# Kernel tuning notes

Hardware: AMD Instinct MI355X
Metric: run time of the kernel (lower is better)

The kernel has to match this reference:

```python
import jax, jax.numpy as jnp
import numpy as np

N_NODES = 20000
N_REL = 200
DIM = 128
N_EDGES = 200000
N_TIMES = 8


def setup_inputs() -> dict:
    key = jax.random.key(0)
    ks = jax.random.split(key, 12)
    s = 1.0 / np.sqrt(DIM)
    return {
        "edge_index": jax.random.randint(ks[0], (2, N_EDGES), 0, N_NODES),
        "edge_type": jax.random.randint(ks[1], (N_EDGES,), 0, N_REL),
        "edge_time": jax.random.randint(ks[2], (N_EDGES,), 0, N_TIMES),
        "edge_weight": jax.random.uniform(ks[3], (N_EDGES,), dtype=jnp.float32),
        "node_emb": jax.random.normal(ks[4], (N_NODES, DIM), dtype=jnp.float32),
        "rel_emb": jax.random.normal(ks[5], (N_REL, DIM), dtype=jnp.float32),
        "W_enc": jax.random.normal(ks[6], (DIM, DIM), dtype=jnp.float32) * s,
        "Wz": jax.random.normal(ks[7], (DIM, DIM), dtype=jnp.float32) * s,
        "Uz": jax.random.normal(ks[8], (DIM, DIM), dtype=jnp.float32) * s,
        "Wh": jax.random.normal(ks[9], (DIM, DIM), dtype=jnp.float32) * s,
        "Uh": jax.random.normal(ks[10], (DIM, DIM), dtype=jnp.float32) * s,
        "bz": jnp.zeros((DIM,), dtype=jnp.float32),
        "bh": jnp.zeros((DIM,), dtype=jnp.float32),
        "num_times": N_TIMES,
    }


def reference(edge_index, edge_type, edge_time, edge_weight,
              node_emb, rel_emb, W_enc, Wz, Uz, Wh, Uh, bz, bh, num_times):
    # TemporalEncoder.forward: loop over sorted unique timestamps; per-step
    # masked-edge GNN encode (R-GCN lite) then gated SSM cell; state detached.
    src, dst = edge_index[0], edge_index[1]
    rel_e = rel_emb[edge_type]          # [E, D] gather (constant across steps)
    src_e = node_emb[src]               # [E, D]
    n_nodes = node_emb.shape[0]

    def step(state, t):
        m = (edge_time == t).astype(edge_weight.dtype)       # [E]
        msg = src_e * rel_e * (edge_weight * m)[:, None]     # [E, D]
        agg = jax.ops.segment_sum(msg, dst, num_segments=n_nodes)  # [N, D]
        h = jnp.tanh(agg @ W_enc)                            # base_encoder output
        z = jax.nn.sigmoid(h @ Wz + state @ Uz + bz)
        cand = jnp.tanh(h @ Wh + state @ Uh + bh)
        new_state = (1.0 - z) * state + z * cand             # ssm.cell
        return jax.lax.stop_gradient(new_state), new_state   # state.detach()

    state0 = jnp.zeros_like(node_emb)
    _, outs = jax.lax.scan(step, state0, jnp.arange(num_times))
    return outs[-1]  # last_out, shape [N, D]
```

## Files before the change

kernel.cpp:

```cpp
#include <hip/hip_runtime.h>

#define N_NODES 20000
#define N_REL 200
#define N_EDGES 200000
#define DIM 128
#define T_STEPS 8
#define N_TILES (N_NODES / 16)
#define KEYS (N_NODES * T_STEPS)
#define SCAN_N (KEYS + 1)
#define SCAN_BLKS ((SCAN_N + 1023) / 1024)

typedef short short8 __attribute__((ext_vector_type(8)));
typedef float f32x4 __attribute__((ext_vector_type(4)));

static __device__ __forceinline__ unsigned short f2bf(float f) {
  union { float f; unsigned u; } v; v.f = f;
  unsigned r = v.u + 0x7fffu + ((v.u >> 16) & 1u);
  return (unsigned short)(r >> 16);
}
static __device__ __forceinline__ unsigned cvt_pk_bf16(float lo, float hi) {
  unsigned r;
  asm("v_cvt_pk_bf16_f32 %0, %1, %2" : "=v"(r) : "v"(lo), "v"(hi));
  return r;
}
static __device__ __forceinline__ float fast_tanh(float x) {
  float e = __expf(2.f * x);
  return 1.f - 2.f / (e + 1.f);
}
static __device__ __forceinline__ float fast_sig(float x) {
  return 1.f / (1.f + __expf(-x));
}

__global__ void repack5(const float* __restrict__ w0,
                        const float* __restrict__ w1,
                        const float* __restrict__ w2,
                        const float* __restrict__ w3,
                        const float* __restrict__ w4,
                        unsigned short* __restrict__ pack) {
  int i = blockIdx.x * blockDim.x + threadIdx.x;
  if (i >= 5 * 16384) return;
  int m = i >> 14, r = i & 16383;
  int j = r & 7, lane = (r >> 3) & 63, ks = (r >> 9) & 3, nt = (r >> 11) & 7;
  int n = nt * 16 + (lane & 15);
  int k = ks * 32 + (lane >> 4) * 8 + j;
  const float* w = (m == 0) ? w0 : (m == 1) ? w1 : (m == 2) ? w2
                 : (m == 3) ? w3 : w4;
  pack[i] = f2bf(w[k * DIM + n]);
}

__global__ void hist_k(const int* __restrict__ dst, const int* __restrict__ etime,
                       int* __restrict__ counts) {
  int i = blockIdx.x * blockDim.x + threadIdx.x;
  if (i >= N_EDGES) return;
  atomicAdd(&counts[dst[i] * T_STEPS + etime[i]], 1);
}

__global__ void scan1_k(const int* __restrict__ counts,
                        int* __restrict__ base, int* __restrict__ bsum) {
  __shared__ int ls[256];
  int tid = threadIdx.x;
  int i0 = blockIdx.x * 1024 + tid * 4;
  int v[4], ts = 0;
#pragma unroll
  for (int r = 0; r < 4; r++) {
    v[r] = (i0 + r < SCAN_N) ? counts[i0 + r] : 0;
    ts += v[r];
  }
  ls[tid] = ts; __syncthreads();
#pragma unroll
  for (int off = 1; off < 256; off <<= 1) {
    int x = (tid >= off) ? ls[tid - off] : 0;
    __syncthreads(); ls[tid] += x; __syncthreads();
  }
  int run = ls[tid] - ts;
  if (tid == 255) bsum[blockIdx.x] = ls[255];
#pragma unroll
  for (int r = 0; r < 4; r++) {
    if (i0 + r < SCAN_N) base[i0 + r] = run;
    run += v[r];
  }
}

__global__ void scan2_k(int* __restrict__ bsum) {
  __shared__ int ls[256];
  int tid = threadIdx.x;
  int v = (tid < SCAN_BLKS) ? bsum[tid] : 0;
  ls[tid] = v; __syncthreads();
#pragma unroll
  for (int off = 1; off < 256; off <<= 1) {
    int x = (tid >= off) ? ls[tid - off] : 0;
    __syncthreads(); ls[tid] += x; __syncthreads();
  }
  if (tid < SCAN_BLKS) bsum[tid] = ls[tid] - v;
}

__global__ void fill_k(const int* __restrict__ src, const int* __restrict__ dst,
                       const int* __restrict__ etype, const int* __restrict__ etime,
                       const float* __restrict__ ew,
                       const int* __restrict__ base, const int* __restrict__ bsum,
                       int* __restrict__ cursor, uint2* __restrict__ ep2) {
  int i = blockIdx.x * blockDim.x + threadIdx.x;
  if (i >= N_EDGES) return;
  int key = dst[i] * T_STEPS + etime[i];
  int pos = base[key] + bsum[key >> 10] + atomicAdd(&cursor[key], 1);
  uint2 e;
  e.x = (unsigned)src[i] | ((unsigned)etype[i] << 15);
  e.y = __float_as_uint(ew[i]);
  ep2[pos] = e;
}

__launch_bounds__(512, 4)
__global__ void fused_recur(const int* __restrict__ base,
                            const int* __restrict__ bsum,
                            const uint2* __restrict__ ep2,
                            const float* __restrict__ nemb,
                            const float* __restrict__ remb,
                            const unsigned short* __restrict__ pack,
                            const float* __restrict__ bz,
                            const float* __restrict__ bh,
                            float* __restrict__ out) {
  __shared__ unsigned short aggL[T_STEPS * 16 * 136];
  __shared__ unsigned short Hb[2][16 * 136];
  __shared__ unsigned short Sb[2][16 * 136];
  int lane = threadIdx.x & 63;
  int nt = threadIdx.x >> 6;
  int q = lane >> 4, l15 = lane & 15;
  int row0 = blockIdx.x * 16;
  int c = nt * 16 + l15;

#pragma unroll
  for (int ln = 0; ln < 2; ln++) {
    int nl = nt * 2 + ln;
    int kb = (row0 + nl) * T_STEPS;
    int prev = base[kb] + bsum[kb >> 10];
#pragma unroll
    for (int tt = 0; tt < T_STEPS; tt++) {
      int kn = kb + tt + 1;
      int e1 = base[kn] + bsum[kn >> 10];
      float ax = 0.f, ay = 0.f;
      for (int i = prev; i < e1; i++) {
        uint2 e = ep2[i];
        float w = __uint_as_float(e.y);
        int s = e.x & 0x7fff, rt = e.x >> 15;
        float2 sv = ((const float2*)(nemb + (size_t)s * DIM))[lane];
        float2 rv = ((const float2*)(remb + (size_t)rt * DIM))[lane];
        ax += sv.x * rv.x * w;
        ay += sv.y * rv.y * w;
      }
      prev = e1;
      ((unsigned*)&aggL[(tt * 16 + nl) * 136])[lane] = cvt_pk_bf16(ax, ay);
    }
  }
  __syncthreads();

  unsigned hpk[T_STEPS][2];
  {
    short8 wenc[4];
#pragma unroll
    for (int ks = 0; ks < 4; ks++)
      wenc[ks] = *(const short8*)(pack + ((nt * 4 + ks) * 64 + lane) * 8);
#pragma unroll
    for (int t = 0; t < T_STEPS; t++) {
      f32x4 acch = (f32x4){0.f, 0.f, 0.f, 0.f};
#pragma unroll
      for (int ks = 0; ks < 4; ks++) {
        short8 aA = *(const short8*)&aggL[(t * 16 + l15) * 136 + ks * 32 + q * 8];
        acch = __builtin_amdgcn_mfma_f32_16x16x32_bf16(aA, wenc[ks], acch, 0, 0, 0);
      }
      hpk[t][0] = cvt_pk_bf16(fast_tanh(acch[0]), fast_tanh(acch[1]));
      hpk[t][1] = cvt_pk_bf16(fast_tanh(acch[2]), fast_tanh(acch[3]));
    }
  }

  short8 wz[4], uz[4], wh[4], uh[4];
#pragma unroll
  for (int ks = 0; ks < 4; ks++) {
    int fo = ((nt * 4 + ks) * 64 + lane) * 8;
    wz[ks] = *(const short8*)(pack + 16384 * 1 + fo);
    uz[ks] = *(const short8*)(pack + 16384 * 2 + fo);
    wh[ks] = *(const short8*)(pack + 16384 * 3 + fo);
    uh[ks] = *(const short8*)(pack + 16384 * 4 + fo);
  }
  float bzv = bz[c];
  float bhv = bh[c];

  f32x4 stC = (f32x4){0.f, 0.f, 0.f, 0.f};

#pragma unroll
  for (int t = 0; t < T_STEPS; t++) {
    unsigned short* hB = Hb[t & 1];
    unsigned short* sB = Sb[t & 1];
    unsigned s01 = cvt_pk_bf16(stC[0], stC[1]);
    unsigned s23 = cvt_pk_bf16(stC[2], stC[3]);
    hB[(q * 4 + 0) * 136 + c] = (unsigned short)hpk[t][0];
    hB[(q * 4 + 1) * 136 + c] = (unsigned short)(hpk[t][0] >> 16);
    hB[(q * 4 + 2) * 136 + c] = (unsigned short)hpk[t][1];
    hB[(q * 4 + 3) * 136 + c] = (unsigned short)(hpk[t][1] >> 16);
    sB[(q * 4 + 0) * 136 + c] = (unsigned short)s01;
    sB[(q * 4 + 1) * 136 + c] = (unsigned short)(s01 >> 16);
    sB[(q * 4 + 2) * 136 + c] = (unsigned short)s23;
    sB[(q * 4 + 3) * 136 + c] = (unsigned short)(s23 >> 16);
    __syncthreads();

    f32x4 accz = (f32x4){bzv, bzv, bzv, bzv};
    f32x4 accc = (f32x4){bhv, bhv, bhv, bhv};
#pragma unroll
    for (int ks = 0; ks < 4; ks++) {
      short8 hA = *(const short8*)&hB[l15 * 136 + ks * 32 + q * 8];
      short8 sA = *(const short8*)&sB[l15 * 136 + ks * 32 + q * 8];
      accz = __builtin_amdgcn_mfma_f32_16x16x32_bf16(hA, wz[ks], accz, 0, 0, 0);
      accz = __builtin_amdgcn_mfma_f32_16x16x32_bf16(sA, uz[ks], accz, 0, 0, 0);
      accc = __builtin_amdgcn_mfma_f32_16x16x32_bf16(hA, wh[ks], accc, 0, 0, 0);
      accc = __builtin_amdgcn_mfma_f32_16x16x32_bf16(sA, uh[ks], accc, 0, 0, 0);
    }
#pragma unroll
    for (int r = 0; r < 4; r++) {
      float z = fast_sig(accz[r]);
      float cc = fast_tanh(accc[r]);
      stC[r] = (1.f - z) * stC[r] + z * cc;
    }
  }

#pragma unroll
  for (int r = 0; r < 4; r++)
    out[(size_t)(row0 + q * 4 + r) * DIM + c] = stC[r];
}

extern "C" void kernel_launch(void* const* d_in, const int* in_sizes, int n_in,
                              void* d_out, int out_size, void* d_ws, size_t ws_size,
                              hipStream_t stream) {
  const int* eidx  = (const int*)d_in[0];
  const int* src   = eidx;
  const int* dst   = eidx + N_EDGES;
  const int* etype = (const int*)d_in[1];
  const int* etime = (const int*)d_in[2];
  const float* ew   = (const float*)d_in[3];
  const float* nemb = (const float*)d_in[4];
  const float* remb = (const float*)d_in[5];
  const float* Wenc = (const float*)d_in[6];
  const float* Wz   = (const float*)d_in[7];
  const float* Uz   = (const float*)d_in[8];
  const float* Wh   = (const float*)d_in[9];
  const float* Uh   = (const float*)d_in[10];
  const float* bz   = (const float*)d_in[11];
  const float* bh   = (const float*)d_in[12];

  int* counts = (int*)d_ws;
  int* cursor = counts + SCAN_N;
  int* bsum   = cursor + KEYS;
  int* base   = bsum + 256;
  uint2* ep2  = (uint2*)(base + ((SCAN_N + 1) & ~1));
  unsigned short* pack = (unsigned short*)(ep2 + N_EDGES);
  float* outp = (float*)d_out;

  hipMemsetAsync(counts, 0, (size_t)(SCAN_N + KEYS) * sizeof(int), stream);
  repack5<<<(5 * 16384 + 255) / 256, 256, 0, stream>>>(Wenc, Wz, Uz, Wh, Uh, pack);
  hist_k<<<(N_EDGES + 255) / 256, 256, 0, stream>>>(dst, etime, counts);
  scan1_k<<<SCAN_BLKS, 256, 0, stream>>>(counts, base, bsum);
  scan2_k<<<1, 256, 0, stream>>>(bsum);
  fill_k<<<(N_EDGES + 255) / 256, 256, 0, stream>>>(src, dst, etype, etime, ew,
                                                    base, bsum, cursor, ep2);
  fused_recur<<<N_TILES, 512, 0, stream>>>(base, bsum, ep2, nemb, remb,
                                           pack, bz, bh, outp);
}
```

Baseline: 213.1 us.

## Replace CSR sort with fixed-capacity per-tile edge buckets

Drops the histogram, two-level scan and sorted fill, replacing them with one atomic append of each edge into a fixed 512-slot bucket per 16-node tile, with time and local row packed into the edge word. The recurrence kernel now scans the whole tile bucket in every wave, skips edges that belong to other waves, and accumulates into per-timestep register arrays through predicated adds. This removes the memset and several launch and scan passes. In exchange every wave reads all edges of its tile and keeps more registers live, and edges beyond the capacity are silently dropped, which only works if no tile exceeds 512 edges (the mean here is about 160).

```diff
diff --git a/kernel.cpp b/kernel.cpp
--- a/kernel.cpp
+++ b/kernel.cpp
@@ -6,9 +6,7 @@
 #define DIM 128
 #define T_STEPS 8
 #define N_TILES (N_NODES / 16)
-#define KEYS (N_NODES * T_STEPS)
-#define SCAN_N (KEYS + 1)
-#define SCAN_BLKS ((SCAN_N + 1023) / 1024)
+#define CAP 512
 
 typedef short short8 __attribute__((ext_vector_type(8)));
 typedef float f32x4 __attribute__((ext_vector_type(4)));
@@ -36,8 +34,10 @@
                         const float* __restrict__ w2,
                         const float* __restrict__ w3,
                         const float* __restrict__ w4,
-                        unsigned short* __restrict__ pack) {
+                        unsigned short* __restrict__ pack,
+                        int* __restrict__ cursor) {
   int i = blockIdx.x * blockDim.x + threadIdx.x;
+  if (i < N_TILES) cursor[i] = 0;
   if (i >= 5 * 16384) return;
   int m = i >> 14, r = i & 16383;
   int j = r & 7, lane = (r >> 3) & 63, ks = (r >> 9) & 3, nt = (r >> 11) & 7;
@@ -48,71 +48,27 @@
   pack[i] = f2bf(w[k * DIM + n]);
 }
 
-__global__ void hist_k(const int* __restrict__ dst, const int* __restrict__ etime,
-                       int* __restrict__ counts) {
+__global__ void binfill_k(const int* __restrict__ src, const int* __restrict__ dst,
+                          const int* __restrict__ etype, const int* __restrict__ etime,
+                          const float* __restrict__ ew,
+                          int* __restrict__ cursor, uint2* __restrict__ bkt) {
   int i = blockIdx.x * blockDim.x + threadIdx.x;
   if (i >= N_EDGES) return;
-  atomicAdd(&counts[dst[i] * T_STEPS + etime[i]], 1);
-}
-
-__global__ void scan1_k(const int* __restrict__ counts,
-                        int* __restrict__ base, int* __restrict__ bsum) {
-  __shared__ int ls[256];
-  int tid = threadIdx.x;
-  int i0 = blockIdx.x * 1024 + tid * 4;
-  int v[4], ts = 0;
-#pragma unroll
-  for (int r = 0; r < 4; r++) {
-    v[r] = (i0 + r < SCAN_N) ? counts[i0 + r] : 0;
-    ts += v[r];
-  }
-  ls[tid] = ts; __syncthreads();
-#pragma unroll
-  for (int off = 1; off < 256; off <<= 1) {
-    int x = (tid >= off) ? ls[tid - off] : 0;
-    __syncthreads(); ls[tid] += x; __syncthreads();
-  }
-  int run = ls[tid] - ts;
-  if (tid == 255) bsum[blockIdx.x] = ls[255];
-#pragma unroll
-  for (int r = 0; r < 4; r++) {
-    if (i0 + r < SCAN_N) base[i0 + r] = run;
-    run += v[r];
-  }
-}
-
-__global__ void scan2_k(int* __restrict__ bsum) {
-  __shared__ int ls[256];
-  int tid = threadIdx.x;
-  int v = (tid < SCAN_BLKS) ? bsum[tid] : 0;
-  ls[tid] = v; __syncthreads();
-#pragma unroll
-  for (int off = 1; off < 256; off <<= 1) {
-    int x = (tid >= off) ? ls[tid - off] : 0;
-    __syncthreads(); ls[tid] += x; __syncthreads();
-  }
-  if (tid < SCAN_BLKS) bsum[tid] = ls[tid] - v;
-}
-
-__global__ void fill_k(const int* __restrict__ src, const int* __restrict__ dst,
-                       const int* __restrict__ etype, const int* __restrict__ etime,
-                       const float* __restrict__ ew,
-                       const int* __restrict__ base, const int* __restrict__ bsum,
-                       int* __restrict__ cursor, uint2* __restrict__ ep2) {
-  int i = blockIdx.x * blockDim.x + threadIdx.x;
-  if (i >= N_EDGES) return;
-  int key = dst[i] * T_STEPS + etime[i];
-  int pos = base[key] + bsum[key >> 10] + atomicAdd(&cursor[key], 1);
-  uint2 e;
-  e.x = (unsigned)src[i] | ((unsigned)etype[i] << 15);
-  e.y = __float_as_uint(ew[i]);
-  ep2[pos] = e;
+  int d = dst[i];
+  int tile = d >> 4;
+  int pos = atomicAdd(&cursor[tile], 1);
+  if (pos < CAP) {
+    uint2 e;
+    e.x = (unsigned)src[i] | ((unsigned)etype[i] << 15)
+        | ((unsigned)etime[i] << 23) | ((unsigned)(d & 15) << 26);
+    e.y = __float_as_uint(ew[i]);
+    bkt[(size_t)tile * CAP + pos] = e;
+  }
 }
 
 __launch_bounds__(512, 4)
-__global__ void fused_recur(const int* __restrict__ base,
-                            const int* __restrict__ bsum,
-                            const uint2* __restrict__ ep2,
+__global__ void fused_recur(const int* __restrict__ cursor,
+                            const uint2* __restrict__ bkt,
                             const float* __restrict__ nemb,
                             const float* __restrict__ remb,
                             const unsigned short* __restrict__ pack,
@@ -125,30 +81,46 @@
   int lane = threadIdx.x & 63;
   int nt = threadIdx.x >> 6;
   int q = lane >> 4, l15 = lane & 15;
-  int row0 = blockIdx.x * 16;
+  int tile = blockIdx.x;
+  int row0 = tile * 16;
   int c = nt * 16 + l15;
 
-#pragma unroll
-  for (int ln = 0; ln < 2; ln++) {
-    int nl = nt * 2 + ln;
-    int kb = (row0 + nl) * T_STEPS;
-    int prev = base[kb] + bsum[kb >> 10];
+  {
+    int cnt = cursor[tile];
+    if (cnt > CAP) cnt = CAP;
+    const uint2* bp = bkt + (size_t)tile * CAP;
+    float ax0[T_STEPS], ay0[T_STEPS], ax1[T_STEPS], ay1[T_STEPS];
 #pragma unroll
     for (int tt = 0; tt < T_STEPS; tt++) {
-      int kn = kb + tt + 1;
-      int e1 = base[kn] + bsum[kn >> 10];
-      float ax = 0.f, ay = 0.f;
-      for (int i = prev; i < e1; i++) {
-        uint2 e = ep2[i];
+      ax0[tt] = 0.f; ay0[tt] = 0.f; ax1[tt] = 0.f; ay1[tt] = 0.f;
+    }
+    for (int i = 0; i < cnt; i++) {
+      uint2 e = bp[i];
+      int nl = (int)(e.x >> 26);
+      if ((nl >> 1) == nt) {
+        int s = e.x & 0x7fff, rt = (e.x >> 15) & 0xff, t = (e.x >> 23) & 7;
         float w = __uint_as_float(e.y);
-        int s = e.x & 0x7fff, rt = e.x >> 15;
         float2 sv = ((const float2*)(nemb + (size_t)s * DIM))[lane];
         float2 rv = ((const float2*)(remb + (size_t)rt * DIM))[lane];
-        ax += sv.x * rv.x * w;
-        ay += sv.y * rv.y * w;
+        float m0 = sv.x * rv.x * w;
+        float m1 = sv.y * rv.y * w;
+        bool odd = nl & 1;
+        float e00 = odd ? 0.f : m0, e01 = odd ? 0.f : m1;
+        float e10 = odd ? m0 : 0.f, e11 = odd ? m1 : 0.f;
+#pragma unroll
+        for (int tt = 0; tt < T_STEPS; tt++) {
+          bool h = (t == tt);
+          ax0[tt] += h ? e00 : 0.f;
+          ay0[tt] += h ? e01 : 0.f;
+          ax1[tt] += h ? e10 : 0.f;
+          ay1[tt] += h ? e11 : 0.f;
+        }
       }
-      prev = e1;
-      ((unsigned*)&aggL[(tt * 16 + nl) * 136])[lane] = cvt_pk_bf16(ax, ay);
+    }
+#pragma unroll
+    for (int tt = 0; tt < T_STEPS; tt++) {
+      ((unsigned*)&aggL[(tt * 16 + nt * 2 + 0) * 136])[lane] = cvt_pk_bf16(ax0[tt], ay0[tt]);
+      ((unsigned*)&aggL[(tt * 16 + nt * 2 + 1) * 136])[lane] = cvt_pk_bf16(ax1[tt], ay1[tt]);
     }
   }
   __syncthreads();
@@ -245,21 +217,15 @@
   const float* bz   = (const float*)d_in[11];
   const float* bh   = (const float*)d_in[12];
 
-  int* counts = (int*)d_ws;
-  int* cursor = counts + SCAN_N;
-  int* bsum   = cursor + KEYS;
-  int* base   = bsum + 256;
-  uint2* ep2  = (uint2*)(base + ((SCAN_N + 1) & ~1));
-  unsigned short* pack = (unsigned short*)(ep2 + N_EDGES);
+  int* cursor = (int*)d_ws;
+  uint2* bkt  = (uint2*)(cursor + ((N_TILES + 1) & ~1));
+  unsigned short* pack = (unsigned short*)(bkt + (size_t)N_TILES * CAP);
   float* outp = (float*)d_out;
 
-  hipMemsetAsync(counts, 0, (size_t)(SCAN_N + KEYS) * sizeof(int), stream);
-  repack5<<<(5 * 16384 + 255) / 256, 256, 0, stream>>>(Wenc, Wz, Uz, Wh, Uh, pack);
-  hist_k<<<(N_EDGES + 255) / 256, 256, 0, stream>>>(dst, etime, counts);
-  scan1_k<<<SCAN_BLKS, 256, 0, stream>>>(counts, base, bsum);
-  scan2_k<<<1, 256, 0, stream>>>(bsum);
-  fill_k<<<(N_EDGES + 255) / 256, 256, 0, stream>>>(src, dst, etype, etime, ew,
-                                                    base, bsum, cursor, ep2);
-  fused_recur<<<N_TILES, 512, 0, stream>>>(base, bsum, ep2, nemb, remb,
+  repack5<<<(5 * 16384 + 255) / 256, 256, 0, stream>>>(Wenc, Wz, Uz, Wh, Uh,
+                                                       pack, cursor);
+  binfill_k<<<(N_EDGES + 255) / 256, 256, 0, stream>>>(src, dst, etype, etime,
+                                                       ew, cursor, bkt);
+  fused_recur<<<N_TILES, 512, 0, stream>>>(cursor, bkt, nemb, remb,
                                            pack, bz, bh, outp);
 }
```

New measurement: 239.0 us. +12.2%, slower.

## Interleave two node gathers per wavefront and split recurrent MFMA chains

Applied to the files above, without the earlier changes.

The edge-gather phase now preloads all CSR bounds for the wavefront's two nodes and walks both nodes' edge lists in one interleaved loop, so their independent global loads can be in flight together instead of running as two serial chains. The recurrent GRU step splits each gate accumulation into separate h-path and state-path accumulators, which shortens dependent MFMA chains. It also skips the state MFMAs, the state LDS stores and the state LDS reads at t=0, where the state is zero. The interleaved loop adds branch divergence when the two lists differ in length, and the extra accumulators raise register pressure.

```diff
diff --git a/kernel.cpp b/kernel.cpp
--- a/kernel.cpp
+++ b/kernel.cpp
@@ -125,30 +125,46 @@
   int lane = threadIdx.x & 63;
   int nt = threadIdx.x >> 6;
   int q = lane >> 4, l15 = lane & 15;
-  int row0 = blockIdx.x * 16;
+  int tile = blockIdx.x;
+  int row0 = tile * 16;
   int c = nt * 16 + l15;
 
-#pragma unroll
-  for (int ln = 0; ln < 2; ln++) {
-    int nl = nt * 2 + ln;
-    int kb = (row0 + nl) * T_STEPS;
-    int prev = base[kb] + bsum[kb >> 10];
+  {
+    int kb = (row0 + nt * 2) * T_STEPS;
+    int b0[9], b1[9];
+#pragma unroll
+    for (int k = 0; k < 9; k++) {
+      int k0 = kb + k, k1 = kb + T_STEPS + k;
+      b0[k] = base[k0] + bsum[k0 >> 10];
+      b1[k] = base[k1] + bsum[k1 >> 10];
+    }
+    int i0 = b0[0], i1 = b1[0];
 #pragma unroll
     for (int tt = 0; tt < T_STEPS; tt++) {
-      int kn = kb + tt + 1;
-      int e1 = base[kn] + bsum[kn >> 10];
-      float ax = 0.f, ay = 0.f;
-      for (int i = prev; i < e1; i++) {
-        uint2 e = ep2[i];
-        float w = __uint_as_float(e.y);
-        int s = e.x & 0x7fff, rt = e.x >> 15;
-        float2 sv = ((const float2*)(nemb + (size_t)s * DIM))[lane];
-        float2 rv = ((const float2*)(remb + (size_t)rt * DIM))[lane];
-        ax += sv.x * rv.x * w;
-        ay += sv.y * rv.y * w;
+      int e0 = b0[tt + 1], e1 = b1[tt + 1];
+      float ax0 = 0.f, ay0 = 0.f, ax1 = 0.f, ay1 = 0.f;
+      while (i0 < e0 || i1 < e1) {
+        if (i0 < e0) {
+          uint2 e = ep2[i0++];
+          float w = __uint_as_float(e.y);
+          int s = e.x & 0x7fff, rt = e.x >> 15;
+          float2 sv = ((const float2*)(nemb + (size_t)s * DIM))[lane];
+          float2 rv = ((const float2*)(remb + (size_t)rt * DIM))[lane];
+          ax0 += sv.x * rv.x * w;
+          ay0 += sv.y * rv.y * w;
+        }
+        if (i1 < e1) {
+          uint2 e = ep2[i1++];
+          float w = __uint_as_float(e.y);
+          int s = e.x & 0x7fff, rt = e.x >> 15;
+          float2 sv = ((const float2*)(nemb + (size_t)s * DIM))[lane];
+          float2 rv = ((const float2*)(remb + (size_t)rt * DIM))[lane];
+          ax1 += sv.x * rv.x * w;
+          ay1 += sv.y * rv.y * w;
+        }
       }
-      prev = e1;
-      ((unsigned*)&aggL[(tt * 16 + nl) * 136])[lane] = cvt_pk_bf16(ax, ay);
+      ((unsigned*)&aggL[(tt * 16 + nt * 2 + 0) * 136])[lane] = cvt_pk_bf16(ax0, ay0);
+      ((unsigned*)&aggL[(tt * 16 + nt * 2 + 1) * 136])[lane] = cvt_pk_bf16(ax1, ay1);
     }
   }
   __syncthreads();
@@ -190,33 +206,50 @@
   for (int t = 0; t < T_STEPS; t++) {
     unsigned short* hB = Hb[t & 1];
     unsigned short* sB = Sb[t & 1];
-    unsigned s01 = cvt_pk_bf16(stC[0], stC[1]);
-    unsigned s23 = cvt_pk_bf16(stC[2], stC[3]);
     hB[(q * 4 + 0) * 136 + c] = (unsigned short)hpk[t][0];
     hB[(q * 4 + 1) * 136 + c] = (unsigned short)(hpk[t][0] >> 16);
     hB[(q * 4 + 2) * 136 + c] = (unsigned short)hpk[t][1];
     hB[(q * 4 + 3) * 136 + c] = (unsigned short)(hpk[t][1] >> 16);
-    sB[(q * 4 + 0) * 136 + c] = (unsigned short)s01;
-    sB[(q * 4 + 1) * 136 + c] = (unsigned short)(s01 >> 16);
-    sB[(q * 4 + 2) * 136 + c] = (unsigned short)s23;
-    sB[(q * 4 + 3) * 136 + c] = (unsigned short)(s23 >> 16);
+    if (t > 0) {
+      unsigned s01 = cvt_pk_bf16(stC[0], stC[1]);
+      unsigned s23 = cvt_pk_bf16(stC[2], stC[3]);
+      sB[(q * 4 + 0) * 136 + c] = (unsigned short)s01;
+      sB[(q * 4 + 1) * 136 + c] = (unsigned short)(s01 >> 16);
+      sB[(q * 4 + 2) * 136 + c] = (unsigned short)s23;
+      sB[(q * 4 + 3) * 136 + c] = (unsigned short)(s23 >> 16);
+    }
     __syncthreads();
 
-    f32x4 accz = (f32x4){bzv, bzv, bzv, bzv};
-    f32x4 accc = (f32x4){bhv, bhv, bhv, bhv};
+    short8 hA[4], sA[4];
+#pragma unroll
+    for (int ks = 0; ks < 4; ks++)
+      hA[ks] = *(const short8*)&hB[l15 * 136 + ks * 32 + q * 8];
+    if (t > 0) {
+#pragma unroll
+      for (int ks = 0; ks < 4; ks++)
+        sA[ks] = *(const short8*)&sB[l15 * 136 + ks * 32 + q * 8];
+    }
+
+    f32x4 zh = (f32x4){bzv, bzv, bzv, bzv};
+    f32x4 ch = (f32x4){bhv, bhv, bhv, bhv};
+    f32x4 zs = (f32x4){0.f, 0.f, 0.f, 0.f};
+    f32x4 cs = (f32x4){0.f, 0.f, 0.f, 0.f};
 #pragma unroll
     for (int ks = 0; ks < 4; ks++) {
-      short8 hA = *(const short8*)&hB[l15 * 136 + ks * 32 + q * 8];
-      short8 sA = *(const short8*)&sB[l15 * 136 + ks * 32 + q * 8];
-      accz = __builtin_amdgcn_mfma_f32_16x16x32_bf16(hA, wz[ks], accz, 0, 0, 0);
-      accz = __builtin_amdgcn_mfma_f32_16x16x32_bf16(sA, uz[ks], accz, 0, 0, 0);
-      accc = __builtin_amdgcn_mfma_f32_16x16x32_bf16(hA, wh[ks], accc, 0, 0, 0);
-      accc = __builtin_amdgcn_mfma_f32_16x16x32_bf16(sA, uh[ks], accc, 0, 0, 0);
+      zh = __builtin_amdgcn_mfma_f32_16x16x32_bf16(hA[ks], wz[ks], zh, 0, 0, 0);
+      ch = __builtin_amdgcn_mfma_f32_16x16x32_bf16(hA[ks], wh[ks], ch, 0, 0, 0);
+    }
+    if (t > 0) {
+#pragma unroll
+      for (int ks = 0; ks < 4; ks++) {
+        zs = __builtin_amdgcn_mfma_f32_16x16x32_bf16(sA[ks], uz[ks], zs, 0, 0, 0);
+        cs = __builtin_amdgcn_mfma_f32_16x16x32_bf16(sA[ks], uh[ks], cs, 0, 0, 0);
+      }
     }
 #pragma unroll
     for (int r = 0; r < 4; r++) {
-      float z = fast_sig(accz[r]);
-      float cc = fast_tanh(accc[r]);
+      float z = fast_sig(zh[r] + zs[r]);
+      float cc = fast_tanh(ch[r] + cs[r]);
       stC[r] = (1.f - z) * stC[r] + z * cc;
     }
   }
```

Result: no change. 214.2 us (+0.5%).

## Precompute input-side gate projections for all steps outside the serial recurrence

Applied to the files above, without the earlier changes.

The h@Wz and h@Wh products for all timesteps are now computed in a batched pre-pass, with h stored back into the agg shared buffer, before the sequential state loop. The recurrent loop then only runs the state@Uz and state@Uh MFMAs. Step 0 is peeled because the state starts at zero, which removes its barrier and state MFMAs, and the separate H shared buffer is dropped. Keeping the precomputed accumulators in registers raises register pressure, so the occupancy hint falls from 4 to 3 blocks per CU.

```diff
diff --git a/kernel.cpp b/kernel.cpp
--- a/kernel.cpp
+++ b/kernel.cpp
@@ -109,7 +109,7 @@
   ep2[pos] = e;
 }
 
-__launch_bounds__(512, 4)
+__launch_bounds__(512, 3)
 __global__ void fused_recur(const int* __restrict__ base,
                             const int* __restrict__ bsum,
                             const uint2* __restrict__ ep2,
@@ -120,12 +120,12 @@
                             const float* __restrict__ bh,
                             float* __restrict__ out) {
   __shared__ unsigned short aggL[T_STEPS * 16 * 136];
-  __shared__ unsigned short Hb[2][16 * 136];
   __shared__ unsigned short Sb[2][16 * 136];
   int lane = threadIdx.x & 63;
   int nt = threadIdx.x >> 6;
   int q = lane >> 4, l15 = lane & 15;
-  int row0 = blockIdx.x * 16;
+  int tile = blockIdx.x;
+  int row0 = tile * 16;
   int c = nt * 16 + l15;
 
 #pragma unroll
@@ -171,52 +171,91 @@
       hpk[t][1] = cvt_pk_bf16(fast_tanh(acch[2]), fast_tanh(acch[3]));
     }
   }
-
-  short8 wz[4], uz[4], wh[4], uh[4];
+  __syncthreads();
+
+#pragma unroll
+  for (int t = 0; t < T_STEPS; t++) {
+    int rbase = (t * 16 + q * 4) * 136 + c;
+    aggL[rbase + 0 * 136] = (unsigned short)hpk[t][0];
+    aggL[rbase + 1 * 136] = (unsigned short)(hpk[t][0] >> 16);
+    aggL[rbase + 2 * 136] = (unsigned short)hpk[t][1];
+    aggL[rbase + 3 * 136] = (unsigned short)(hpk[t][1] >> 16);
+  }
+  __syncthreads();
+
+  f32x4 zh[T_STEPS], ch[T_STEPS];
+  {
+    short8 wzf[4], whf[4];
+#pragma unroll
+    for (int ks = 0; ks < 4; ks++) {
+      int fo = ((nt * 4 + ks) * 64 + lane) * 8;
+      wzf[ks] = *(const short8*)(pack + 16384 * 1 + fo);
+      whf[ks] = *(const short8*)(pack + 16384 * 3 + fo);
+    }
+    float bzv = bz[c];
+    float bhv = bh[c];
+#pragma unroll
+    for (int t = 0; t < T_STEPS; t++) {
+      short8 hA[4];
+#pragma unroll
+      for (int ks = 0; ks < 4; ks++)
+        hA[ks] = *(const short8*)&aggL[(t * 16 + l15) * 136 + ks * 32 + q * 8];
+      f32x4 az = (f32x4){bzv, bzv, bzv, bzv};
+      f32x4 ac = (f32x4){bhv, bhv, bhv, bhv};
+#pragma unroll
+      for (int ks = 0; ks < 4; ks++) {
+        az = __builtin_amdgcn_mfma_f32_16x16x32_bf16(hA[ks], wzf[ks], az, 0, 0, 0);
+        ac = __builtin_amdgcn_mfma_f32_16x16x32_bf16(hA[ks], whf[ks], ac, 0, 0, 0);
+      }
+      zh[t] = az;
+      ch[t] = ac;
+    }
+  }
+
+  short8 uz[4], uh[4];
 #pragma unroll
   for (int ks = 0; ks < 4; ks++) {
     int fo = ((nt * 4 + ks) * 64 + lane) * 8;
-    wz[ks] = *(const short8*)(pack + 16384 * 1 + fo);
     uz[ks] = *(const short8*)(pack + 16384 * 2 + fo);
-    wh[ks] = *(const short8*)(pack + 16384 * 3 + fo);
     uh[ks] = *(const short8*)(pack + 16384 * 4 + fo);
   }
-  float bzv = bz[c];
-  float bhv = bh[c];
-
-  f32x4 stC = (f32x4){0.f, 0.f, 0.f, 0.f};
-
-#pragma unroll
-  for (int t = 0; t < T_STEPS; t++) {
-    unsigned short* hB = Hb[t & 1];
+
+  f32x4 stC;
+#pragma unroll
+  for (int r = 0; r < 4; r++) {
+    float z = fast_sig(zh[0][r]);
+    float cc = fast_tanh(ch[0][r]);
+    stC[r] = z * cc;
+  }
+
+#pragma unroll
+  for (int t = 1; t < T_STEPS; t++) {
     unsigned short* sB = Sb[t & 1];
     unsigned s01 = cvt_pk_bf16(stC[0], stC[1]);
     unsigned s23 = cvt_pk_bf16(stC[2], stC[3]);
-    hB[(q * 4 + 0) * 136 + c] = (unsigned short)hpk[t][0];
-    hB[(q * 4 + 1) * 136 + c] = (unsigned short)(hpk[t][0] >> 16);
-    hB[(q * 4 + 2) * 136 + c] = (unsigned short)hpk[t][1];
-    hB[(q * 4 + 3) * 136 + c] = (unsigned short)(hpk[t][1] >> 16);
-    sB[(q * 4 + 0) * 136 + c] = (unsigned short)s01;
-    sB[(q * 4 + 1) * 136 + c] = (unsigned short)(s01 >> 16);
-    sB[(q * 4 + 2) * 136 + c] = (unsigned short)s23;
-    sB[(q * 4 + 3) * 136 + c] = (unsigned short)(s23 >> 16);
+    int rbase = (q * 4) * 136 + c;
+    sB[rbase + 0 * 136] = (unsigned short)s01;
+    sB[rbase + 1 * 136] = (unsigned short)(s01 >> 16);
+    sB[rbase + 2 * 136] = (unsigned short)s23;
+    sB[rbase + 3 * 136] = (unsigned short)(s23 >> 16);
     __syncthreads();
 
-    f32x4 accz = (f32x4){bzv, bzv, bzv, bzv};
-    f32x4 accc = (f32x4){bhv, bhv, bhv, bhv};
+    short8 sA[4];
+#pragma unroll
+    for (int ks = 0; ks < 4; ks++)
+      sA[ks] = *(const short8*)&sB[l15 * 136 + ks * 32 + q * 8];
+
+    f32x4 zs = (f32x4){0.f, 0.f, 0.f, 0.f};
+    f32x4 cs = (f32x4){0.f, 0.f, 0.f, 0.f};
 #pragma unroll
     for (int ks = 0; ks < 4; ks++) {
-      short8 hA = *(const short8*)&hB[l15 * 136 + ks * 32 + q * 8];
-      short8 sA = *(const short8*)&sB[l15 * 136 + ks * 32 + q * 8];
-      accz = __builtin_amdgcn_mfma_f32_16x16x32_bf16(hA, wz[ks], accz, 0, 0, 0);
-      accz = __builtin_amdgcn_mfma_f32_16x16x32_bf16(sA, uz[ks], accz, 0, 0, 0);
-      accc = __builtin_amdgcn_mfma_f32_16x16x32_bf16(hA, wh[ks], accc, 0, 0, 0);
-      accc = __builtin_amdgcn_mfma_f32_16x16x32_bf16(sA, uh[ks], accc, 0, 0, 0);
+      zs = __builtin_amdgcn_mfma_f32_16x16x32_bf16(sA[ks], uz[ks], zs, 0, 0, 0);
+      cs = __builtin_amdgcn_mfma_f32_16x16x32_bf16(sA[ks], uh[ks], cs, 0, 0, 0);
     }
 #pragma unroll
     for (int r = 0; r < 4; r++) {
-      float z = fast_sig(accz[r]);
-      float cc = fast_tanh(accc[r]);
+      float z = fast_sig(zh[t][r] + zs[r]);
+      float cc = fast_tanh(ch[t][r] + cs[r]);
       stC[r] = (1.f - z) * stC[r] + z * cc;
     }
   }
```

Result: slower. 253.4 us (+18.9%).
